# Performance work log

Measured on AMD Instinct MI355X. Metric: run time of the kernel, lower is better.

Reference implementation:

```python
import jax, jax.numpy as jnp
import numpy as np
import math

NUM_HEADS = 8
Q_STRIDE = 2
KV_STRIDE = 2
POS_MAG = 1.0
WAVE_LEN = 1000.0


def _pos_embedding(h, w, h_kv, w_kv, feat_dim):
    # sinusoidal embedding of coordinate differences (in input-resolution units)
    h_idxs = jnp.arange(h, dtype=jnp.float32) * Q_STRIDE
    w_idxs = jnp.arange(w, dtype=jnp.float32) * Q_STRIDE
    h_kv_idxs = jnp.arange(h_kv, dtype=jnp.float32) * KV_STRIDE
    w_kv_idxs = jnp.arange(w_kv, dtype=jnp.float32) * KV_STRIDE
    h_diff = (h_idxs[:, None] - h_kv_idxs[None, :]) * POS_MAG  # [h, h_kv]
    w_diff = (w_idxs[:, None] - w_kv_idxs[None, :]) * POS_MAG  # [w, w_kv]
    feat_range = jnp.arange(feat_dim // 4, dtype=jnp.float32)
    dim_mat = WAVE_LEN ** (4.0 / feat_dim * feat_range)       # [feat_dim/4]
    ang_x = w_diff[:, :, None] / dim_mat                       # [w, w_kv, feat_dim/4]
    ang_y = h_diff[:, :, None] / dim_mat                       # [h, h_kv, feat_dim/4]
    emb_x = jnp.concatenate([jnp.sin(ang_x), jnp.cos(ang_x)], axis=2)  # [w, w_kv, feat_dim/2]
    emb_y = jnp.concatenate([jnp.sin(ang_y), jnp.cos(ang_y)], axis=2)  # [h, h_kv, feat_dim/2]
    return emb_x, emb_y


def setup_inputs() -> dict:
    key = jax.random.key(0)
    ks = jax.random.split(key, 10)
    n, C, H, W = 2, 256, 96, 96
    s = 0.05
    return {
        "x": jax.random.normal(ks[0], (n, C, H, W), jnp.float32),
        "Wq": jax.random.normal(ks[1], (C, C), jnp.float32) * s,
        "Wk": jax.random.normal(ks[2], (C, C), jnp.float32) * s,
        "Wv": jax.random.normal(ks[3], (C, C), jnp.float32) * s,
        "Wx": jax.random.normal(ks[4], (C, C // 2), jnp.float32) * s,
        "Wy": jax.random.normal(ks[5], (C, C // 2), jnp.float32) * s,
        "appr_bias": jax.random.normal(ks[6], (C,), jnp.float32) * s,
        "Wp": jax.random.normal(ks[7], (C, C), jnp.float32) * s,
        "bp": jax.random.normal(ks[8], (C,), jnp.float32) * s,
        "gamma": jax.random.normal(ks[9], (1,), jnp.float32),
    }


def reference(x, Wq, Wk, Wv, Wx, Wy, appr_bias, Wp, bp, gamma):
    n, C, H, W = x.shape
    g = NUM_HEADS
    d = C // g  # qk_embed_dim == v_dim
    # AvgPool2d(kernel_size=1, stride=s) == strided subsampling
    x_q = x[:, :, ::Q_STRIDE, ::Q_STRIDE]
    x_kv = x[:, :, ::KV_STRIDE, ::KV_STRIDE]
    h, w = x_q.shape[2], x_q.shape[3]
    h_kv, w_kv = x_kv.shape[2], x_kv.shape[3]

    # 1x1 convs (no bias) == channel matmuls
    q = jnp.einsum('oc,nchw->nohw', Wq, x_q)   # [n, C, h, w]
    k = jnp.einsum('oc,nchw->nohw', Wk, x_kv)  # [n, C, h_kv, w_kv]
    v = jnp.einsum('oc,nchw->nohw', Wv, x_kv)  # [n, C, h_kv, w_kv]

    emb_x, emb_y = _pos_embedding(h, w, h_kv, w_kv, C)
    inv_sqrt2 = 1.0 / math.sqrt(2.0)
    # Linear(feat_dim/2 -> C), split into heads, scale by 1/sqrt(2)
    pos_x = (jnp.einsum('wvf,of->wvo', emb_x, Wx).reshape(w, w_kv, g, d)
             .transpose(2, 0, 1, 3)) * inv_sqrt2  # [g, w, w_kv, d]
    pos_y = (jnp.einsum('huf,of->huo', emb_y, Wy).reshape(h, h_kv, g, d)
             .transpose(2, 0, 1, 3)) * inv_sqrt2  # [g, h, h_kv, d]

    qr = q.reshape(n, g, d, h, w).transpose(0, 1, 3, 4, 2)  # [n, g, h, w, d]
    kr = k.reshape(n, g, d, h_kv * w_kv)                     # [n, g, d, kv]

    # bias . key term, broadcast over query positions
    e_key = jnp.einsum('gd,ngdk->ngk', appr_bias.reshape(g, d), kr)
    e_key = e_key.reshape(n, g, 1, 1, h_kv, w_kv)
    # query . pos_x term (broadcast over h_kv), query . pos_y term (broadcast over w_kv)
    e_x = jnp.einsum('nghwd,gwvd->nghwv', qr, pos_x)[:, :, :, :, None, :]
    e_y = jnp.einsum('nghwd,ghud->nghwu', qr, pos_y)[:, :, :, :, :, None]

    energy = (e_key + e_x + e_y).reshape(n, g, h * w, h_kv * w_kv)
    attn = jax.nn.softmax(energy, axis=-1)  # [n, g, hw, kv]

    vr = v.reshape(n, g, d, h_kv * w_kv)  # [n, g, d, kv]
    out = jnp.einsum('ngqk,ngdk->ngdq', attn, vr).reshape(n, C, h, w)

    out = jnp.einsum('oc,nchw->nohw', Wp, out) + bp[None, :, None, None]
    out = jax.image.resize(out, (n, C, H, W), method='bilinear')
    return gamma * out + x
```

## Files before the change

### kernel.cpp

```cpp
#include <hip/hip_runtime.h>
#include <hip/hip_bf16.h>
#include <math.h>

#define NB 2
#define CC 256
#define NPOS 2304
#define NDELTA 95

typedef __attribute__((ext_vector_type(8))) short short8;
typedef __attribute__((ext_vector_type(4))) float floatx4;

__device__ inline unsigned short f2bf(float x) {
    unsigned int u = __float_as_uint(x);
    u = (u + 0x7FFFu + ((u >> 16) & 1u)) >> 16;
    return (unsigned short)u;
}
__device__ inline float bf2f(unsigned short h) {
    return __uint_as_float(((unsigned int)h) << 16);
}
__device__ inline unsigned int pk2(float a, float b) {
    return (unsigned int)f2bf(a) | ((unsigned int)f2bf(b) << 16);
}
__device__ inline unsigned int pkmul(unsigned int a, unsigned int b) {
    __hip_bfloat162 x = *(__hip_bfloat162*)&a;
    __hip_bfloat162 y = *(__hip_bfloat162*)&b;
    __hip_bfloat162 r = __hmul2(x, y);
    return *(unsigned int*)&r;
}

__global__ __launch_bounds__(256) void prep_extract_kernel(
    const float* __restrict__ Wx, const float* __restrict__ Wy,
    const float* __restrict__ Wk, const float* __restrict__ ab,
    const float* __restrict__ Wq, const float* __restrict__ Wv,
    const float* __restrict__ Wp, const float* __restrict__ x,
    unsigned short* __restrict__ posxb, unsigned short* __restrict__ posyb,
    unsigned short* __restrict__ Wb, unsigned short* __restrict__ Wpb,
    unsigned short* __restrict__ xs_t)
{
    __shared__ __align__(16) unsigned short Lt[64][264];
    int b = blockIdx.x;
    int t = threadIdx.x;
    if (b < NDELTA) {
        float* emb = (float*)&Lt[0][0];
        float delta = (float)(b - 47);
        if (t < 64) {
            float dim_inv = exp2f(-(float)t * 0.15571537944784511f);
            float ang = 2.0f * delta * dim_inv;
            emb[t]      = sinf(ang);
            emb[t + 64] = cosf(ang);
        }
        __syncthreads();
        float sx = 0.f, sy = 0.f;
        const float* wxr = Wx + t * 128;
        const float* wyr = Wy + t * 128;
        for (int f = 0; f < 128; ++f) {
            float e = emb[f];
            sx += e * wxr[f];
            sy += e * wyr[f];
        }
        const float inv_sqrt2 = 0.70710678118654752440f;
        int g = t >> 5, d = t & 31;
        posxb[((size_t)g * 96 + b) * 32 + d] = f2bf(sx * inv_sqrt2);
        posyb[((size_t)g * 96 + b) * 32 + d] = f2bf(sy * inv_sqrt2);
    } else if (b == NDELTA) {
        int g = t >> 5, d = t & 31;
        posxb[((size_t)g * 96 + 95) * 32 + d] = 0;
        posyb[((size_t)g * 96 + 95) * 32 + d] = 0;
    } else if (b < 96 + 640) {
        int o = b - 96;
        float v = 0.f;
        if (o < 256)      v = Wq[o * 256 + t];
        else if (o < 512) v = Wv[(o - 256) * 256 + t];
        else if (o < 520) {
            int g = o - 512;
            float s = 0.f;
            for (int d = 0; d < 32; ++d)
                s += ab[g * 32 + d] * Wk[(g * 32 + d) * 256 + t];
            v = s;
        }
        Wb[(size_t)o * 256 + t] = f2bf(v);
    } else if (b < 992) {
        int o = b - 736;
        Wpb[(size_t)o * 256 + t] = f2bf(Wp[o * 256 + t]);
    } else {
        int blk = b - 992;
        int pt = blk % 36;
        int n = blk / 36;
        int p0 = pt * 64;
        int cw = t >> 4;
        int pl = t & 15;

        for (int cc = 0; cc < 16; ++cc) {
            int c = cc * 16 + cw;
            const float* src = x + ((size_t)(n * 256 + c)) * (96 * 96);
            #pragma unroll
            for (int k = 0; k < 4; ++k) {
                int p = p0 + pl + k * 16;
                int i = p / 48, j = p - i * 48;
                Lt[pl + k * 16][c] = f2bf(src[(2 * i) * 96 + 2 * j]);
            }
        }
        __syncthreads();
        #pragma unroll
        for (int it = 0; it < 8; ++it) {
            int s = t + it * 256;
            int p = s >> 5, c8 = s & 31;
            uint4 v = *(const uint4*)&Lt[p][c8 * 8];
            *(uint4*)(xs_t + ((size_t)(n * NPOS + p0 + p)) * 256 + c8 * 8) = v;
        }
    }
}

__global__ __launch_bounds__(256, 2) void qkv_kernel(
    const unsigned short* __restrict__ xs_t, const unsigned short* __restrict__ Wb,
    unsigned short* __restrict__ qbuf, float* __restrict__ vbuf,
    float* __restrict__ ek)
{
    int mT = blockIdx.x;
    int nT = blockIdx.y;
    int t = threadIdx.x;
    int wm = t >> 6, L = t & 63, l16 = L & 15, oct = L >> 4;
    int colBase = nT * 64;
    int n = colBase / NPOS;
    int p0 = colBase - n * NPOS;
    int o_w = mT * 128 + wm * 32;

    const unsigned short* A0 = Wb + (size_t)(o_w + l16) * 256 + oct * 8;
    const unsigned short* A1 = A0 + 16 * 256;
    const unsigned short* B0 = xs_t + ((size_t)(n * NPOS + p0 + l16)) * 256 + oct * 8;

    floatx4 acc[2][4] = {};
    #pragma unroll
    for (int kc = 0; kc < 8; ++kc) {
        int k0 = kc * 32;
        short8 a0 = *(const short8*)(A0 + k0);
        short8 a1 = *(const short8*)(A1 + k0);
        short8 b0 = *(const short8*)(B0 + k0);
        short8 b1 = *(const short8*)(B0 + 16 * 256 + k0);
        short8 b2 = *(const short8*)(B0 + 32 * 256 + k0);
        short8 b3 = *(const short8*)(B0 + 48 * 256 + k0);
        acc[0][0] = __builtin_amdgcn_mfma_f32_16x16x32_bf16(a0, b0, acc[0][0], 0, 0, 0);
        acc[0][1] = __builtin_amdgcn_mfma_f32_16x16x32_bf16(a0, b1, acc[0][1], 0, 0, 0);
        acc[0][2] = __builtin_amdgcn_mfma_f32_16x16x32_bf16(a0, b2, acc[0][2], 0, 0, 0);
        acc[0][3] = __builtin_amdgcn_mfma_f32_16x16x32_bf16(a0, b3, acc[0][3], 0, 0, 0);
        acc[1][0] = __builtin_amdgcn_mfma_f32_16x16x32_bf16(a1, b0, acc[1][0], 0, 0, 0);
        acc[1][1] = __builtin_amdgcn_mfma_f32_16x16x32_bf16(a1, b1, acc[1][1], 0, 0, 0);
        acc[1][2] = __builtin_amdgcn_mfma_f32_16x16x32_bf16(a1, b2, acc[1][2], 0, 0, 0);
        acc[1][3] = __builtin_amdgcn_mfma_f32_16x16x32_bf16(a1, b3, acc[1][3], 0, 0, 0);
    }

    if (o_w < 256) {
        #pragma unroll
        for (int af = 0; af < 2; ++af) {
            int ob = o_w + af * 16 + oct * 4;
            int g = ob >> 5, d0 = ob & 31;
            #pragma unroll
            for (int f = 0; f < 4; ++f) {
                int p = p0 + f * 16 + l16;
                uint2 w;
                w.x = pk2(acc[af][f][0], acc[af][f][1]);
                w.y = pk2(acc[af][f][2], acc[af][f][3]);
                *(uint2*)&qbuf[((size_t)(n * 8 + g) * NPOS + p) * 32 + d0] = w;
            }
        }
    } else if (o_w < 512) {
        #pragma unroll
        for (int af = 0; af < 2; ++af) {
            #pragma unroll
            for (int f = 0; f < 4; ++f) {
                int p = p0 + f * 16 + l16;
                #pragma unroll
                for (int r = 0; r < 4; ++r) {
                    int o = o_w + af * 16 + oct * 4 + r;
                    vbuf[((size_t)(n * 256 + (o - 256))) * NPOS + p] = acc[af][f][r];
                }
            }
        }
    } else {
        #pragma unroll
        for (int af = 0; af < 2; ++af) {
            #pragma unroll
            for (int f = 0; f < 4; ++f) {
                int p = p0 + f * 16 + l16;
                #pragma unroll
                for (int r = 0; r < 4; ++r) {
                    int o = o_w + af * 16 + oct * 4 + r;
                    if (o < 520)
                        ek[((size_t)(n * 8 + (o - 512))) * NPOS + p] = acc[af][f][r];
                }
            }
        }
    }
}

__global__ __launch_bounds__(256) void vhat_kernel(
    const float* __restrict__ vbuf, const float* __restrict__ ek,
    uint4* __restrict__ vhat)
{
    int tile = blockIdx.x;
    int ng = blockIdx.y;
    int k0 = tile * 96;
    int t = threadIdx.x;
    const float* vb = vbuf + (size_t)ng * 32 * NPOS;
    uint4* out = vhat + ((size_t)ng * 24 + tile) * 576;

    __shared__ __align__(16) float Ae[96];
    if (t < 96) Ae[t] = __expf(ek[(size_t)ng * NPOS + k0 + t]);
    __syncthreads();

    for (int s = t; s < 576; s += 256) {
        int grp = s >> 6;
        int Ls = s & 63;
        int cc = grp / 3;
        int nn = grp - cc * 3;
        int koct = cc * 32 + ((Ls >> 4) << 3);
        uint4 w = make_uint4(0u, 0u, 0u, 0u);
        if (nn < 2) {
            int d = nn * 16 + (Ls & 15);
            const float* vp = vb + (size_t)d * NPOS + k0 + koct;
            const float* ap = Ae + koct;
            float4 v0 = *(const float4*)vp;
            float4 v1 = *(const float4*)(vp + 4);
            float4 a0 = *(const float4*)ap;
            float4 a1 = *(const float4*)(ap + 4);
            w.x = pk2(v0.x * a0.x, v0.y * a0.y);
            w.y = pk2(v0.z * a0.z, v0.w * a0.w);
            w.z = pk2(v1.x * a1.x, v1.y * a1.y);
            w.w = pk2(v1.z * a1.z, v1.w * a1.w);
        } else if ((Ls & 15) == 0) {
            const float* ap = Ae + koct;
            float4 a0 = *(const float4*)ap;
            float4 a1 = *(const float4*)(ap + 4);
            w.x = pk2(a0.x, a0.y);
            w.y = pk2(a0.z, a0.w);
            w.z = pk2(a1.x, a1.y);
            w.w = pk2(a1.z, a1.w);
        }
        out[s] = w;
    }
}

#define DO_TILE(BB, TT) do {                                                   \
    int u0_ = (TT) * 2;                                                        \
    unsigned int y0_ = Ys[qp * 50 + u0_];     y0_ |= y0_ << 16;                \
    unsigned int y1_ = Ys[qp * 50 + u0_ + 1]; y1_ |= y1_ << 16;                \
    unsigned int Yc0_ = y0_, Yc1_ = (o < 2) ? y0_ : y1_, Yc2_ = y1_;           \
    union { unsigned int u[4]; short8 s; } av_;                                \
    av_.u[0] = pkmul(Xp[0], Yc0_); av_.u[1] = pkmul(Xp[1], Yc0_);              \
    av_.u[2] = pkmul(Xp[2], Yc0_); av_.u[3] = pkmul(Xp[3], Yc0_);              \
    acc0 = __builtin_amdgcn_mfma_f32_16x16x32_bf16(av_.s, *(const short8*)&BB[0], acc0, 0, 0, 0); \
    acc1 = __builtin_amdgcn_mfma_f32_16x16x32_bf16(av_.s, *(const short8*)&BB[1], acc1, 0, 0, 0); \
    acc2 = __builtin_amdgcn_mfma_f32_16x16x32_bf16(av_.s, *(const short8*)&BB[2], acc2, 0, 0, 0); \
    av_.u[0] = pkmul(Xp[4], Yc1_); av_.u[1] = pkmul(Xp[5], Yc1_);              \
    av_.u[2] = pkmul(Xp[6], Yc1_); av_.u[3] = pkmul(Xp[7], Yc1_);              \
    acc0 = __builtin_amdgcn_mfma_f32_16x16x32_bf16(av_.s, *(const short8*)&BB[3], acc0, 0, 0, 0); \
    acc1 = __builtin_amdgcn_mfma_f32_16x16x32_bf16(av_.s, *(const short8*)&BB[4], acc1, 0, 0, 0); \
    acc2 = __builtin_amdgcn_mfma_f32_16x16x32_bf16(av_.s, *(const short8*)&BB[5], acc2, 0, 0, 0); \
    av_.u[0] = pkmul(Xp[8], Yc2_); av_.u[1] = pkmul(Xp[9], Yc2_);              \
    av_.u[2] = pkmul(Xp[10], Yc2_); av_.u[3] = pkmul(Xp[11], Yc2_);            \
    acc0 = __builtin_amdgcn_mfma_f32_16x16x32_bf16(av_.s, *(const short8*)&BB[6], acc0, 0, 0, 0); \
    acc1 = __builtin_amdgcn_mfma_f32_16x16x32_bf16(av_.s, *(const short8*)&BB[7], acc1, 0, 0, 0); \
    acc2 = __builtin_amdgcn_mfma_f32_16x16x32_bf16(av_.s, *(const short8*)&BB[8], acc2, 0, 0, 0); \
} while (0)

__global__ __launch_bounds__(256, 2) void attn_kernel(
    const unsigned short* __restrict__ qbuf, const unsigned short* __restrict__ posxb,
    const unsigned short* __restrict__ posyb, const uint4* __restrict__ vhat,
    unsigned short* __restrict__ oattn_t)
{
    __shared__ unsigned short Xs[64 * 50];
    __shared__ unsigned short Ys[64 * 50];
    __shared__ float linv_s[64];

    int blk = blockIdx.x;
    int qt = blk % 36;
    int ng = blk / 36;
    int nb = ng >> 3, g = ng & 7;
    int qbase = qt * 64;
    int t = threadIdx.x;
    int m = t >> 6, L = t & 63;
    int l16 = L & 15, oct = L >> 4;

    {
        int qtile0 = qbase + m * 16;
        int hq = qtile0 / 48;
        int wq0 = qtile0 - hq * 48;
        short8 aq = *(const short8*)(qbuf +
            ((size_t)ng * NPOS + qtile0 + l16) * 32 + oct * 8);
        const unsigned short* pxg = posxb + (size_t)g * 96 * 32;
        const unsigned short* pyg = posyb + (size_t)g * 96 * 32;
        floatx4 zero = {0.f, 0.f, 0.f, 0.f};
        #pragma unroll
        for (int j = 0; j < 6; ++j) {
            int dl = j * 16 + l16;
            short8 bx = *(const short8*)(pxg + (size_t)dl * 32 + oct * 8);
            short8 by = *(const short8*)(pyg + (size_t)dl * 32 + oct * 8);
            floatx4 tx = __builtin_amdgcn_mfma_f32_16x16x32_bf16(aq, bx, zero, 0, 0, 0);
            floatx4 ty = __builtin_amdgcn_mfma_f32_16x16x32_bf16(aq, by, zero, 0, 0, 0);
            int u = hq + 47 - dl;
            bool uok = (u >= 0) && (u < 48);
            #pragma unroll
            for (int r = 0; r < 4; ++r) {
                int ql = oct * 4 + r;
                int v = wq0 + ql + 47 - dl;
                if (v >= 0 && v < 48)
                    Xs[(m * 16 + ql) * 50 + v] = f2bf(__expf(tx[r]));
                if (uok)
                    Ys[(m * 16 + ql) * 50 + u] = f2bf(__expf(ty[r]));
            }
        }
    }
    __syncthreads();

    int qp = m * 16 + l16;
    int o = oct;
    unsigned int Xp[12];
    #pragma unroll
    for (int c = 0; c < 3; ++c)
        #pragma unroll
        for (int jj = 0; jj < 4; ++jj) {
            int k = c * 32 + o * 8 + jj * 2;
            int v0 = (k < 48) ? k : k - 48;
            Xp[c * 4 + jj] = *(const unsigned int*)&Xs[qp * 50 + v0];
        }

    floatx4 acc0 = {0.f, 0.f, 0.f, 0.f};
    floatx4 acc1 = {0.f, 0.f, 0.f, 0.f};
    floatx4 acc2 = {0.f, 0.f, 0.f, 0.f};

    const uint4* vb = vhat + (size_t)ng * 24 * 576 + L;
    uint4 Abuf[9], Bbuf[9];
    #pragma unroll
    for (int gg = 0; gg < 9; ++gg) Abuf[gg] = vb[gg * 64];

    for (int tile = 0; tile < 24; tile += 2) {
        const uint4* sB = vb + (tile + 1) * 576;
        #pragma unroll
        for (int gg = 0; gg < 9; ++gg) Bbuf[gg] = sB[gg * 64];
        DO_TILE(Abuf, tile);
        if (tile + 2 < 24) {
            const uint4* sA = vb + (tile + 2) * 576;
            #pragma unroll
            for (int gg = 0; gg < 9; ++gg) Abuf[gg] = sA[gg * 64];
        }
        DO_TILE(Bbuf, tile + 1);
    }

    if ((L & 15) == 0) {
        int qc = m * 16 + (L >> 4) * 4;
        #pragma unroll
        for (int r = 0; r < 4; ++r)
            linv_s[qc + r] = 1.0f / acc2[r];
    }
    __syncthreads();
    {
        int qc = m * 16 + (L >> 4) * 4;
        int d0 = L & 15;
        #pragma unroll
        for (int r = 0; r < 4; ++r) {
            float lir = linv_s[qc + r];
            size_t row = ((size_t)nb * NPOS + qbase + qc + r) * 256;
            oattn_t[row + g * 32 + d0]      = f2bf(acc0[r] * lir);
            oattn_t[row + g * 32 + 16 + d0] = f2bf(acc1[r] * lir);
        }
    }
}

__global__ __launch_bounds__(256, 2) void proj_kernel(
    const unsigned short* __restrict__ oattn_t, const unsigned short* __restrict__ Wpb,
    const float* __restrict__ bpv, unsigned short* __restrict__ projb)
{
    int mT = blockIdx.x;
    int nT = blockIdx.y;
    int t = threadIdx.x;
    int wm = t >> 6, L = t & 63, l16 = L & 15, oct = L >> 4;
    int colBase = nT * 64;
    int n = colBase / NPOS;
    int p0 = colBase - n * NPOS;
    int o_w = mT * 128 + wm * 32;

    const unsigned short* A0 = Wpb + (size_t)(o_w + l16) * 256 + oct * 8;
    const unsigned short* A1 = A0 + 16 * 256;
    const unsigned short* B0 = oattn_t + ((size_t)(n * NPOS + p0 + l16)) * 256 + oct * 8;

    floatx4 acc[2][4] = {};
    #pragma unroll
    for (int kc = 0; kc < 8; ++kc) {
        int k0 = kc * 32;
        short8 a0 = *(const short8*)(A0 + k0);
        short8 a1 = *(const short8*)(A1 + k0);
        short8 b0 = *(const short8*)(B0 + k0);
        short8 b1 = *(const short8*)(B0 + 16 * 256 + k0);
        short8 b2 = *(const short8*)(B0 + 32 * 256 + k0);
        short8 b3 = *(const short8*)(B0 + 48 * 256 + k0);
        acc[0][0] = __builtin_amdgcn_mfma_f32_16x16x32_bf16(a0, b0, acc[0][0], 0, 0, 0);
        acc[0][1] = __builtin_amdgcn_mfma_f32_16x16x32_bf16(a0, b1, acc[0][1], 0, 0, 0);
        acc[0][2] = __builtin_amdgcn_mfma_f32_16x16x32_bf16(a0, b2, acc[0][2], 0, 0, 0);
        acc[0][3] = __builtin_amdgcn_mfma_f32_16x16x32_bf16(a0, b3, acc[0][3], 0, 0, 0);
        acc[1][0] = __builtin_amdgcn_mfma_f32_16x16x32_bf16(a1, b0, acc[1][0], 0, 0, 0);
        acc[1][1] = __builtin_amdgcn_mfma_f32_16x16x32_bf16(a1, b1, acc[1][1], 0, 0, 0);
        acc[1][2] = __builtin_amdgcn_mfma_f32_16x16x32_bf16(a1, b2, acc[1][2], 0, 0, 0);
        acc[1][3] = __builtin_amdgcn_mfma_f32_16x16x32_bf16(a1, b3, acc[1][3], 0, 0, 0);
    }

    #pragma unroll
    for (int af = 0; af < 2; ++af) {
        #pragma unroll
        for (int f = 0; f < 4; ++f) {
            int p = p0 + f * 16 + l16;
            #pragma unroll
            for (int r = 0; r < 4; ++r) {
                int o = o_w + af * 16 + oct * 4 + r;
                projb[((size_t)(n * 256 + o)) * NPOS + p] = f2bf(acc[af][f][r] + bpv[o]);
            }
        }
    }
}

__global__ __launch_bounds__(256) void resize_kernel(
    const unsigned short* __restrict__ projb, const float* __restrict__ x,
    const float* __restrict__ gamma, float* __restrict__ out)
{
    int idx4 = blockIdx.x * 256 + threadIdx.x;
    int J0 = (idx4 % 24) * 4;
    int tmp = idx4 / 24;
    int I = tmp % 96;
    int nc = tmp / 96;

    int jr = I >> 1;
    int r0, r1; float w0, w1;
    if ((I & 1) == 0) { r0 = (jr > 0) ? jr - 1 : 0; r1 = jr; w0 = 0.25f; w1 = 0.75f; }
    else              { r0 = jr; r1 = (jr < 47) ? jr + 1 : 47; w0 = 0.75f; w1 = 0.25f; }

    const unsigned short* P = projb + (size_t)nc * NPOS;
    size_t base = ((size_t)nc * 96 + I) * 96 + J0;
    float4 xv = *(const float4*)(x + base);
    float gm = gamma[0];
    float4 ov;
    #pragma unroll
    for (int k = 0; k < 4; ++k) {
        int J = J0 + k;
        int jc = J >> 1;
        int c0, c1; float u0, u1;
        if ((J & 1) == 0) { c0 = (jc > 0) ? jc - 1 : 0; c1 = jc; u0 = 0.25f; u1 = 0.75f; }
        else              { c0 = jc; c1 = (jc < 47) ? jc + 1 : 47; u0 = 0.75f; u1 = 0.25f; }
        float v = w0 * (u0 * bf2f(P[r0 * 48 + c0]) + u1 * bf2f(P[r0 * 48 + c1])) +
                  w1 * (u0 * bf2f(P[r1 * 48 + c0]) + u1 * bf2f(P[r1 * 48 + c1]));
        float xr = (k == 0) ? xv.x : (k == 1) ? xv.y : (k == 2) ? xv.z : xv.w;
        float o = gm * v + xr;
        if (k == 0) ov.x = o; else if (k == 1) ov.y = o; else if (k == 2) ov.z = o; else ov.w = o;
    }
    *(float4*)(out + base) = ov;
}

extern "C" void kernel_launch(void* const* d_in, const int* in_sizes, int n_in,
                              void* d_out, int out_size, void* d_ws, size_t ws_size,
                              hipStream_t stream)
{
    const float* x     = (const float*)d_in[0];
    const float* Wq    = (const float*)d_in[1];
    const float* Wk    = (const float*)d_in[2];
    const float* Wv    = (const float*)d_in[3];
    const float* Wx    = (const float*)d_in[4];
    const float* Wy    = (const float*)d_in[5];
    const float* ab    = (const float*)d_in[6];
    const float* Wp    = (const float*)d_in[7];
    const float* bp    = (const float*)d_in[8];
    const float* gamma = (const float*)d_in[9];
    float* out = (float*)d_out;

    unsigned short* posxb = (unsigned short*)d_ws;
    unsigned short* posyb  = posxb + 8 * 96 * 32;
    unsigned short* Wb     = posyb + 8 * 96 * 32;
    unsigned short* Wpb    = Wb + (size_t)640 * 256;
    unsigned short* xs_t   = Wpb + (size_t)256 * 256;
    unsigned short* qbuf   = xs_t + (size_t)2 * NPOS * 256;
    unsigned short* oattn_t= qbuf + (size_t)2 * NPOS * 256;
    unsigned short* projb  = oattn_t + (size_t)2 * NPOS * 256;
    float* vbuf  = (float*)(projb + (size_t)2 * NPOS * 256);
    float* ek    = vbuf + (size_t)2 * 256 * NPOS;
    uint4* vhat  = (uint4*)(ek + 16 * NPOS);

    hipLaunchKernelGGL(prep_extract_kernel, dim3(1064), dim3(256), 0, stream,
                       Wx, Wy, Wk, ab, Wq, Wv, Wp, x, posxb, posyb, Wb, Wpb, xs_t);
    hipLaunchKernelGGL(qkv_kernel, dim3(5, 72), dim3(256), 0, stream,
                       xs_t, Wb, qbuf, vbuf, ek);
    hipLaunchKernelGGL(vhat_kernel, dim3(24, 16), dim3(256), 0, stream,
                       vbuf, ek, vhat);
    hipLaunchKernelGGL(attn_kernel, dim3(576), dim3(256), 0, stream,
                       qbuf, posxb, posyb, vhat, oattn_t);
    hipLaunchKernelGGL(proj_kernel, dim3(2, 72), dim3(256), 0, stream,
                       oattn_t, Wpb, bp, projb);
    hipLaunchKernelGGL(resize_kernel, dim3((2 * 256 * 96 * 96) / (256 * 4)), dim3(256), 0, stream,
                       projb, x, gamma, out);
}
```

Measured before the change: 152.9 us.

## Fuse six stage kernels into one cooperative persistent kernel with grid syncs

Converts each stage kernel into a device body indexed by a task id and runs all stages inside one cooperative kernel of 512 blocks, separated by grid-wide barriers. The aim is to remove five kernel launch gaps and the tail drain between stages. If the cooperative launch fails, it falls back to six separate launches. In exchange, every stage runs with a fixed 512-block grid under a launch bound of 2 blocks per CU, which may lower occupancy for the memory-bound stages. The combined kernel's register and shared-memory use is set by its largest stage, and each grid sync adds its own cost.

```diff
diff --git a/kernel.cpp b/kernel.cpp
--- a/kernel.cpp
+++ b/kernel.cpp
@@ -1,6 +1,9 @@
 #include <hip/hip_runtime.h>
 #include <hip/hip_bf16.h>
+#include <hip/hip_cooperative_groups.h>
 #include <math.h>
+
+namespace cg = cooperative_groups;
 
 #define NB 2
 #define CC 256
@@ -28,7 +31,8 @@
     return *(unsigned int*)&r;
 }
 
-__global__ __launch_bounds__(256) void prep_extract_kernel(
+
+__device__ __forceinline__ void stageA_body(int task, int t,
     const float* __restrict__ Wx, const float* __restrict__ Wy,
     const float* __restrict__ Wk, const float* __restrict__ ab,
     const float* __restrict__ Wq, const float* __restrict__ Wv,
@@ -38,11 +42,9 @@
     unsigned short* __restrict__ xs_t)
 {
     __shared__ __align__(16) unsigned short Lt[64][264];
-    int b = blockIdx.x;
-    int t = threadIdx.x;
-    if (b < NDELTA) {
+    if (task < NDELTA) {
         float* emb = (float*)&Lt[0][0];
-        float delta = (float)(b - 47);
+        float delta = (float)(task - 47);
         if (t < 64) {
             float dim_inv = exp2f(-(float)t * 0.15571537944784511f);
             float ang = 2.0f * delta * dim_inv;
@@ -60,14 +62,14 @@
         }
         const float inv_sqrt2 = 0.70710678118654752440f;
         int g = t >> 5, d = t & 31;
-        posxb[((size_t)g * 96 + b) * 32 + d] = f2bf(sx * inv_sqrt2);
-        posyb[((size_t)g * 96 + b) * 32 + d] = f2bf(sy * inv_sqrt2);
-    } else if (b == NDELTA) {
+        posxb[((size_t)g * 96 + task) * 32 + d] = f2bf(sx * inv_sqrt2);
+        posyb[((size_t)g * 96 + task) * 32 + d] = f2bf(sy * inv_sqrt2);
+    } else if (task == NDELTA) {
         int g = t >> 5, d = t & 31;
         posxb[((size_t)g * 96 + 95) * 32 + d] = 0;
         posyb[((size_t)g * 96 + 95) * 32 + d] = 0;
-    } else if (b < 96 + 640) {
-        int o = b - 96;
+    } else if (task < 96 + 640) {
+        int o = task - 96;
         float v = 0.f;
         if (o < 256)      v = Wq[o * 256 + t];
         else if (o < 512) v = Wv[(o - 256) * 256 + t];
@@ -79,17 +81,16 @@
             v = s;
         }
         Wb[(size_t)o * 256 + t] = f2bf(v);
-    } else if (b < 992) {
-        int o = b - 736;
+    } else if (task < 992) {
+        int o = task - 736;
         Wpb[(size_t)o * 256 + t] = f2bf(Wp[o * 256 + t]);
     } else {
-        int blk = b - 992;
+        int blk = task - 992;
         int pt = blk % 36;
         int n = blk / 36;
         int p0 = pt * 64;
         int cw = t >> 4;
         int pl = t & 15;
-
         for (int cc = 0; cc < 16; ++cc) {
             int c = cc * 16 + cw;
             const float* src = x + ((size_t)(n * 256 + c)) * (96 * 96);
@@ -111,14 +112,13 @@
     }
 }
 
-__global__ __launch_bounds__(256, 2) void qkv_kernel(
+__device__ __forceinline__ void stageB_body(int task, int t,
     const unsigned short* __restrict__ xs_t, const unsigned short* __restrict__ Wb,
     unsigned short* __restrict__ qbuf, float* __restrict__ vbuf,
     float* __restrict__ ek)
 {
-    int mT = blockIdx.x;
-    int nT = blockIdx.y;
-    int t = threadIdx.x;
+    int mT = task % 5;
+    int nT = task / 5;
     int wm = t >> 6, L = t & 63, l16 = L & 15, oct = L >> 4;
     int colBase = nT * 64;
     int n = colBase / NPOS;
@@ -193,16 +193,15 @@
     }
 }
 
-__global__ __launch_bounds__(256) void vhat_kernel(
+__device__ __forceinline__ void stageC_body(int task, int t,
     const float* __restrict__ vbuf, const float* __restrict__ ek,
     uint4* __restrict__ vhat)
 {
-    int tile = blockIdx.x;
-    int ng = blockIdx.y;
+    int tile = task % 24;
+    int ng = task / 24;
     int k0 = tile * 96;
-    int t = threadIdx.x;
     const float* vb = vbuf + (size_t)ng * 32 * NPOS;
-    uint4* out = vhat + ((size_t)ng * 24 + tile) * 576;
+    uint4* outv = vhat + ((size_t)ng * 24 + tile) * 576;
 
     __shared__ __align__(16) float Ae[96];
     if (t < 96) Ae[t] = __expf(ek[(size_t)ng * NPOS + k0 + t]);
@@ -236,7 +235,7 @@
             w.z = pk2(a1.x, a1.y);
             w.w = pk2(a1.z, a1.w);
         }
-        out[s] = w;
+        outv[s] = w;
     }
 }
 
@@ -263,7 +262,7 @@
     acc2 = __builtin_amdgcn_mfma_f32_16x16x32_bf16(av_.s, *(const short8*)&BB[8], acc2, 0, 0, 0); \
 } while (0)
 
-__global__ __launch_bounds__(256, 2) void attn_kernel(
+__device__ __forceinline__ void stageD_body(int task, int t,
     const unsigned short* __restrict__ qbuf, const unsigned short* __restrict__ posxb,
     const unsigned short* __restrict__ posyb, const uint4* __restrict__ vhat,
     unsigned short* __restrict__ oattn_t)
@@ -272,12 +271,10 @@
     __shared__ unsigned short Ys[64 * 50];
     __shared__ float linv_s[64];
 
-    int blk = blockIdx.x;
-    int qt = blk % 36;
-    int ng = blk / 36;
+    int qt = task % 36;
+    int ng = task / 36;
     int nb = ng >> 3, g = ng & 7;
     int qbase = qt * 64;
-    int t = threadIdx.x;
     int m = t >> 6, L = t & 63;
     int l16 = L & 15, oct = L >> 4;
 
@@ -366,13 +363,12 @@
     }
 }
 
-__global__ __launch_bounds__(256, 2) void proj_kernel(
+__device__ __forceinline__ void stageE_body(int task, int t,
     const unsigned short* __restrict__ oattn_t, const unsigned short* __restrict__ Wpb,
     const float* __restrict__ bpv, unsigned short* __restrict__ projb)
 {
-    int mT = blockIdx.x;
-    int nT = blockIdx.y;
-    int t = threadIdx.x;
+    int mT = task & 1;
+    int nT = task >> 1;
     int wm = t >> 6, L = t & 63, l16 = L & 15, oct = L >> 4;
     int colBase = nT * 64;
     int n = colBase / NPOS;
@@ -417,11 +413,11 @@
     }
 }
 
-__global__ __launch_bounds__(256) void resize_kernel(
+__device__ __forceinline__ void stageF_body(int task, int t,
     const unsigned short* __restrict__ projb, const float* __restrict__ x,
     const float* __restrict__ gamma, float* __restrict__ out)
 {
-    int idx4 = blockIdx.x * 256 + threadIdx.x;
+    int idx4 = task * 256 + t;
     int J0 = (idx4 % 24) * 4;
     int tmp = idx4 / 24;
     int I = tmp % 96;
@@ -447,10 +443,101 @@
         float v = w0 * (u0 * bf2f(P[r0 * 48 + c0]) + u1 * bf2f(P[r0 * 48 + c1])) +
                   w1 * (u0 * bf2f(P[r1 * 48 + c0]) + u1 * bf2f(P[r1 * 48 + c1]));
         float xr = (k == 0) ? xv.x : (k == 1) ? xv.y : (k == 2) ? xv.z : xv.w;
-        float o = gm * v + xr;
-        if (k == 0) ov.x = o; else if (k == 1) ov.y = o; else if (k == 2) ov.z = o; else ov.w = o;
+        float oo = gm * v + xr;
+        if (k == 0) ov.x = oo; else if (k == 1) ov.y = oo;
+        else if (k == 2) ov.z = oo; else ov.w = oo;
     }
     *(float4*)(out + base) = ov;
+}
+
+__global__ __launch_bounds__(256) void prep_extract_kernel(
+    const float* Wx, const float* Wy, const float* Wk, const float* ab,
+    const float* Wq, const float* Wv, const float* Wp, const float* x,
+    unsigned short* posxb, unsigned short* posyb,
+    unsigned short* Wb, unsigned short* Wpb, unsigned short* xs_t)
+{
+    stageA_body(blockIdx.x, threadIdx.x, Wx, Wy, Wk, ab, Wq, Wv, Wp, x,
+                posxb, posyb, Wb, Wpb, xs_t);
+}
+
+__global__ __launch_bounds__(256, 2) void qkv_kernel(
+    const unsigned short* xs_t, const unsigned short* Wb,
+    unsigned short* qbuf, float* vbuf, float* ek)
+{
+    stageB_body(blockIdx.x, threadIdx.x, xs_t, Wb, qbuf, vbuf, ek);
+}
+
+__global__ __launch_bounds__(256) void vhat_kernel(
+    const float* vbuf, const float* ek, uint4* vhat)
+{
+    stageC_body(blockIdx.x, threadIdx.x, vbuf, ek, vhat);
+}
+
+__global__ __launch_bounds__(256, 2) void attn_kernel(
+    const unsigned short* qbuf, const unsigned short* posxb,
+    const unsigned short* posyb, const uint4* vhat, unsigned short* oattn_t)
+{
+    stageD_body(blockIdx.x, threadIdx.x, qbuf, posxb, posyb, vhat, oattn_t);
+}
+
+__global__ __launch_bounds__(256, 2) void proj_kernel(
+    const unsigned short* oattn_t, const unsigned short* Wpb,
+    const float* bpv, unsigned short* projb)
+{
+    stageE_body(blockIdx.x, threadIdx.x, oattn_t, Wpb, bpv, projb);
+}
+
+__global__ __launch_bounds__(256) void resize_kernel(
+    const unsigned short* projb, const float* x,
+    const float* gamma, float* out)
+{
+    stageF_body(blockIdx.x, threadIdx.x, projb, x, gamma, out);
+}
+
+__global__ __launch_bounds__(256, 2) void mega_kernel(
+    const float* x, const float* Wq, const float* Wk, const float* Wv,
+    const float* Wx, const float* Wy, const float* ab, const float* Wp,
+    const float* bp, const float* gamma, float* out,
+    unsigned short* posxb, unsigned short* posyb,
+    unsigned short* Wb, unsigned short* Wpb,
+    unsigned short* xs_t, unsigned short* qbuf,
+    unsigned short* oattn_t, unsigned short* projb,
+    float* vbuf, float* ek, uint4* vhat)
+{
+    cg::grid_group grid = cg::this_grid();
+    int bid = blockIdx.x;
+    int t = threadIdx.x;
+    int stride = gridDim.x;
+
+    for (int task = bid; task < 1064; task += stride) {
+        __syncthreads();
+        stageA_body(task, t, Wx, Wy, Wk, ab, Wq, Wv, Wp, x,
+                    posxb, posyb, Wb, Wpb, xs_t);
+    }
+    grid.sync();
+
+    for (int task = bid; task < 360; task += stride)
+        stageB_body(task, t, xs_t, Wb, qbuf, vbuf, ek);
+    grid.sync();
+
+    for (int task = bid; task < 384; task += stride) {
+        __syncthreads();
+        stageC_body(task, t, vbuf, ek, vhat);
+    }
+    grid.sync();
+
+    for (int task = bid; task < 576; task += stride) {
+        __syncthreads();
+        stageD_body(task, t, qbuf, posxb, posyb, vhat, oattn_t);
+    }
+    grid.sync();
+
+    for (int task = bid; task < 144; task += stride)
+        stageE_body(task, t, oattn_t, Wpb, bp, projb);
+    grid.sync();
+
+    for (int task = bid; task < 4608; task += stride)
+        stageF_body(task, t, projb, x, gamma, out);
 }
 
 extern "C" void kernel_launch(void* const* d_in, const int* in_sizes, int n_in,
@@ -481,16 +568,29 @@
     float* ek    = vbuf + (size_t)2 * 256 * NPOS;
     uint4* vhat  = (uint4*)(ek + 16 * NPOS);
 
-    hipLaunchKernelGGL(prep_extract_kernel, dim3(1064), dim3(256), 0, stream,
-                       Wx, Wy, Wk, ab, Wq, Wv, Wp, x, posxb, posyb, Wb, Wpb, xs_t);
-    hipLaunchKernelGGL(qkv_kernel, dim3(5, 72), dim3(256), 0, stream,
-                       xs_t, Wb, qbuf, vbuf, ek);
-    hipLaunchKernelGGL(vhat_kernel, dim3(24, 16), dim3(256), 0, stream,
-                       vbuf, ek, vhat);
-    hipLaunchKernelGGL(attn_kernel, dim3(576), dim3(256), 0, stream,
-                       qbuf, posxb, posyb, vhat, oattn_t);
-    hipLaunchKernelGGL(proj_kernel, dim3(2, 72), dim3(256), 0, stream,
-                       oattn_t, Wpb, bp, projb);
-    hipLaunchKernelGGL(resize_kernel, dim3((2 * 256 * 96 * 96) / (256 * 4)), dim3(256), 0, stream,
-                       projb, x, gamma, out);
-}
+    void* args[] = {
+        (void*)&x, (void*)&Wq, (void*)&Wk, (void*)&Wv, (void*)&Wx, (void*)&Wy,
+        (void*)&ab, (void*)&Wp, (void*)&bp, (void*)&gamma, (void*)&out,
+        (void*)&posxb, (void*)&posyb, (void*)&Wb, (void*)&Wpb, (void*)&xs_t,
+        (void*)&qbuf, (void*)&oattn_t, (void*)&projb, (void*)&vbuf, (void*)&ek,
+        (void*)&vhat
+    };
+    hipError_t ce = hipLaunchCooperativeKernel((const void*)mega_kernel,
+                                               dim3(512), dim3(256),
+                                               args, 0, stream);
+    if (ce != hipSuccess) {
+        (void)hipGetLastError();
+        hipLaunchKernelGGL(prep_extract_kernel, dim3(1064), dim3(256), 0, stream,
+                           Wx, Wy, Wk, ab, Wq, Wv, Wp, x, posxb, posyb, Wb, Wpb, xs_t);
+        hipLaunchKernelGGL(qkv_kernel, dim3(360), dim3(256), 0, stream,
+                           xs_t, Wb, qbuf, vbuf, ek);
+        hipLaunchKernelGGL(vhat_kernel, dim3(384), dim3(256), 0, stream,
+                           vbuf, ek, vhat);
+        hipLaunchKernelGGL(attn_kernel, dim3(576), dim3(256), 0, stream,
+                           qbuf, posxb, posyb, vhat, oattn_t);
+        hipLaunchKernelGGL(proj_kernel, dim3(144), dim3(256), 0, stream,
+                           oattn_t, Wpb, bp, projb);
+        hipLaunchKernelGGL(resize_kernel, dim3(4608), dim3(256), 0, stream,
+                           projb, x, gamma, out);
+    }
+}
```

Result: slower. 469.1 us (+206.7%).

## Fuse V projection, key-bias exponent and vhat packing into QKV GEMM

Applied to the files above, without the earlier changes.

Folds the separate vhat kernel into the QKV GEMM. V-tile blocks also compute the bias·key row with extra MFMAs, exponentiate it, scale V, transpose through shared memory and write the packed bf16 vhat layout directly. This removes the fp32 vbuf/ek round trip through global memory and one kernel launch, and drops the fifth block column. The cost is extra MFMAs and a shared-memory transpose in the V blocks.

```diff
diff --git a/kernel.cpp b/kernel.cpp
--- a/kernel.cpp
+++ b/kernel.cpp
@@ -111,11 +111,11 @@
     }
 }
 
-__global__ __launch_bounds__(256, 2) void qkv_kernel(
+__global__ __launch_bounds__(256, 2) void qkvh_kernel(
     const unsigned short* __restrict__ xs_t, const unsigned short* __restrict__ Wb,
-    unsigned short* __restrict__ qbuf, float* __restrict__ vbuf,
-    float* __restrict__ ek)
-{
+    unsigned short* __restrict__ qbuf, uint4* __restrict__ vhat)
+{
+    __shared__ __align__(16) unsigned short Vt[4][33][72];
     int mT = blockIdx.x;
     int nT = blockIdx.y;
     int t = threadIdx.x;
@@ -124,12 +124,16 @@
     int n = colBase / NPOS;
     int p0 = colBase - n * NPOS;
     int o_w = mT * 128 + wm * 32;
+    bool isV = (mT >= 2);
+    int gv = (mT & 1) * 4 + wm;
 
     const unsigned short* A0 = Wb + (size_t)(o_w + l16) * 256 + oct * 8;
     const unsigned short* A1 = A0 + 16 * 256;
+    const unsigned short* AE = Wb + (size_t)(512 + gv) * 256 + oct * 8;
     const unsigned short* B0 = xs_t + ((size_t)(n * NPOS + p0 + l16)) * 256 + oct * 8;
 
     floatx4 acc[2][4] = {};
+    floatx4 accE[4] = {};
     #pragma unroll
     for (int kc = 0; kc < 8; ++kc) {
         int k0 = kc * 32;
@@ -147,96 +151,65 @@
         acc[1][1] = __builtin_amdgcn_mfma_f32_16x16x32_bf16(a1, b1, acc[1][1], 0, 0, 0);
         acc[1][2] = __builtin_amdgcn_mfma_f32_16x16x32_bf16(a1, b2, acc[1][2], 0, 0, 0);
         acc[1][3] = __builtin_amdgcn_mfma_f32_16x16x32_bf16(a1, b3, acc[1][3], 0, 0, 0);
-    }
-
-    if (o_w < 256) {
+        if (isV) {
+            short8 ae = *(const short8*)(AE + k0);
+            accE[0] = __builtin_amdgcn_mfma_f32_16x16x32_bf16(ae, b0, accE[0], 0, 0, 0);
+            accE[1] = __builtin_amdgcn_mfma_f32_16x16x32_bf16(ae, b1, accE[1], 0, 0, 0);
+            accE[2] = __builtin_amdgcn_mfma_f32_16x16x32_bf16(ae, b2, accE[2], 0, 0, 0);
+            accE[3] = __builtin_amdgcn_mfma_f32_16x16x32_bf16(ae, b3, accE[3], 0, 0, 0);
+        }
+    }
+
+    if (!isV) {
         #pragma unroll
         for (int af = 0; af < 2; ++af) {
             int ob = o_w + af * 16 + oct * 4;
-            int g = ob >> 5, d0 = ob & 31;
+            int gq = ob >> 5, d0 = ob & 31;
             #pragma unroll
             for (int f = 0; f < 4; ++f) {
                 int p = p0 + f * 16 + l16;
                 uint2 w;
                 w.x = pk2(acc[af][f][0], acc[af][f][1]);
                 w.y = pk2(acc[af][f][2], acc[af][f][3]);
-                *(uint2*)&qbuf[((size_t)(n * 8 + g) * NPOS + p) * 32 + d0] = w;
+                *(uint2*)&qbuf[((size_t)(n * 8 + gq) * NPOS + p) * 32 + d0] = w;
             }
         }
-    } else if (o_w < 512) {
-        #pragma unroll
-        for (int af = 0; af < 2; ++af) {
-            #pragma unroll
-            for (int f = 0; f < 4; ++f) {
-                int p = p0 + f * 16 + l16;
+    } else {
+        #pragma unroll
+        for (int f = 0; f < 4; ++f) {
+            float e = __expf(accE[f][0]);
+            #pragma unroll
+            for (int af = 0; af < 2; ++af)
                 #pragma unroll
-                for (int r = 0; r < 4; ++r) {
-                    int o = o_w + af * 16 + oct * 4 + r;
-                    vbuf[((size_t)(n * 256 + (o - 256))) * NPOS + p] = acc[af][f][r];
-                }
-            }
-        }
-    } else {
-        #pragma unroll
-        for (int af = 0; af < 2; ++af) {
-            #pragma unroll
-            for (int f = 0; f < 4; ++f) {
-                int p = p0 + f * 16 + l16;
-                #pragma unroll
-                for (int r = 0; r < 4; ++r) {
-                    int o = o_w + af * 16 + oct * 4 + r;
-                    if (o < 520)
-                        ek[((size_t)(n * 8 + (o - 512))) * NPOS + p] = acc[af][f][r];
-                }
-            }
-        }
-    }
-}
-
-__global__ __launch_bounds__(256) void vhat_kernel(
-    const float* __restrict__ vbuf, const float* __restrict__ ek,
-    uint4* __restrict__ vhat)
-{
-    int tile = blockIdx.x;
-    int ng = blockIdx.y;
-    int k0 = tile * 96;
-    int t = threadIdx.x;
-    const float* vb = vbuf + (size_t)ng * 32 * NPOS;
-    uint4* out = vhat + ((size_t)ng * 24 + tile) * 576;
-
-    __shared__ __align__(16) float Ae[96];
-    if (t < 96) Ae[t] = __expf(ek[(size_t)ng * NPOS + k0 + t]);
-    __syncthreads();
-
-    for (int s = t; s < 576; s += 256) {
-        int grp = s >> 6;
-        int Ls = s & 63;
-        int cc = grp / 3;
-        int nn = grp - cc * 3;
-        int koct = cc * 32 + ((Ls >> 4) << 3);
-        uint4 w = make_uint4(0u, 0u, 0u, 0u);
-        if (nn < 2) {
-            int d = nn * 16 + (Ls & 15);
-            const float* vp = vb + (size_t)d * NPOS + k0 + koct;
-            const float* ap = Ae + koct;
-            float4 v0 = *(const float4*)vp;
-            float4 v1 = *(const float4*)(vp + 4);
-            float4 a0 = *(const float4*)ap;
-            float4 a1 = *(const float4*)(ap + 4);
-            w.x = pk2(v0.x * a0.x, v0.y * a0.y);
-            w.y = pk2(v0.z * a0.z, v0.w * a0.w);
-            w.z = pk2(v1.x * a1.x, v1.y * a1.y);
-            w.w = pk2(v1.z * a1.z, v1.w * a1.w);
-        } else if ((Ls & 15) == 0) {
-            const float* ap = Ae + koct;
-            float4 a0 = *(const float4*)ap;
-            float4 a1 = *(const float4*)(ap + 4);
-            w.x = pk2(a0.x, a0.y);
-            w.y = pk2(a0.z, a0.w);
-            w.z = pk2(a1.x, a1.y);
-            w.w = pk2(a1.z, a1.w);
-        }
-        out[s] = w;
+                for (int r = 0; r < 4; ++r)
+                    Vt[wm][af * 16 + oct * 4 + r][f * 16 + l16] =
+                        f2bf(acc[af][f][r] * e);
+            if (oct == 0)
+                Vt[wm][32][f * 16 + l16] = f2bf(e);
+        }
+        __syncthreads();
+
+        int i = L >> 3, j = L & 7;
+        int K = p0 + 8 * i;
+        int tile = K / 96;
+        int rem = K - tile * 96;
+        int cc = rem >> 5;
+        int lhi = (rem & 31) >> 3;
+        uint4* vout = vhat + ((size_t)(n * 8 + gv) * 24 + tile) * 576;
+        #pragma unroll
+        for (int mm = 0; mm < 4; ++mm) {
+            int d = j + 8 * mm;
+            int nn = d >> 4;
+            int Ls = lhi * 16 + (d & 15);
+            uint4 w = *(const uint4*)&Vt[wm][d][8 * i];
+            vout[(cc * 3 + nn) * 64 + Ls] = w;
+        }
+        {
+            uint4 wa = (j == 0) ? *(const uint4*)&Vt[wm][32][8 * i]
+                                : make_uint4(0u, 0u, 0u, 0u);
+            vout[(cc * 3 + 2) * 64 + lhi * 16 + j] = wa;
+            vout[(cc * 3 + 2) * 64 + lhi * 16 + j + 8] = make_uint4(0u, 0u, 0u, 0u);
+        }
     }
 }
 
@@ -477,16 +450,14 @@
     unsigned short* qbuf   = xs_t + (size_t)2 * NPOS * 256;
     unsigned short* oattn_t= qbuf + (size_t)2 * NPOS * 256;
     unsigned short* projb  = oattn_t + (size_t)2 * NPOS * 256;
-    float* vbuf  = (float*)(projb + (size_t)2 * NPOS * 256);
-    float* ek    = vbuf + (size_t)2 * 256 * NPOS;
-    uint4* vhat  = (uint4*)(ek + 16 * NPOS);
+    float* unused_vbuf = (float*)(projb + (size_t)2 * NPOS * 256);
+    float* unused_ek   = unused_vbuf + (size_t)2 * 256 * NPOS;
+    uint4* vhat  = (uint4*)(unused_ek + 16 * NPOS);
 
     hipLaunchKernelGGL(prep_extract_kernel, dim3(1064), dim3(256), 0, stream,
                        Wx, Wy, Wk, ab, Wq, Wv, Wp, x, posxb, posyb, Wb, Wpb, xs_t);
-    hipLaunchKernelGGL(qkv_kernel, dim3(5, 72), dim3(256), 0, stream,
-                       xs_t, Wb, qbuf, vbuf, ek);
-    hipLaunchKernelGGL(vhat_kernel, dim3(24, 16), dim3(256), 0, stream,
-                       vbuf, ek, vhat);
+    hipLaunchKernelGGL(qkvh_kernel, dim3(4, 72), dim3(256), 0, stream,
+                       xs_t, Wb, qbuf, vhat);
     hipLaunchKernelGGL(attn_kernel, dim3(576), dim3(256), 0, stream,
                        qbuf, posxb, posyb, vhat, oattn_t);
     hipLaunchKernelGGL(proj_kernel, dim3(2, 72), dim3(256), 0, stream,
```

New measurement: 150.3 us. Within noise of the previous version (-1.7%).
